# Kernel tuning notes

Measured on AMD Instinct MI355X. Metric: run time of the kernel, lower is better.

The kernel has to match this reference:

```python
import jax, jax.numpy as jnp
import numpy as np

DIM = 2048
ORDER = 4
L_MAX = 2048
BATCH = 4  # must equal ORDER due to broadcast in the original module
SEQ = 2048


def setup_inputs() -> dict:
    key = jax.random.key(0)
    k1, k2 = jax.random.split(key)
    x = jax.random.normal(k1, (BATCH, DIM, SEQ), dtype=jnp.float32)
    kernel = jax.random.normal(k2, (ORDER, DIM, L_MAX), dtype=jnp.float32) * 0.02
    bias = jnp.zeros((DIM,), dtype=jnp.float32)
    return {"x": x, "kernel": kernel, "bias": bias}


def reference(x, kernel, bias):
    # x: (B, dim, L); kernel: (order, dim, l_max); B == order by broadcast
    seq_len = x.shape[-1]
    n = 2 * seq_len  # zero-padded FFT length for linear (causal) convolution
    x_fft = jnp.fft.rfft(x, n=n, axis=-1)            # (B, dim, n//2+1) complex
    kernel_fft = jnp.fft.rfft(kernel, n=n, axis=-1)  # (order, dim, n//2+1)
    y_fft = x_fft * kernel_fft                       # broadcast: B == order
    y = jnp.fft.irfft(y_fft, n=n, axis=-1)[:, :, :seq_len]
    return y + x + bias[None, :, None]
```

## Files before the change

### kernel.cpp

```cpp
#include <hip/hip_runtime.h>

typedef __attribute__((ext_vector_type(8)))  short short8;
typedef __attribute__((ext_vector_type(16))) float f32x16;
typedef unsigned int uint;

#define SEQ   2048
#define KB0   1024
#define KSTR2 1040
#define KB1   (KB0 + KSTR2)
#define ZB    (KB0 + 2 * KSTR2)
#define LDSU  (ZB + 16)
#define EX0   1024
#define EX1   2048

__device__ inline uint pack2(float lo, float hi_) {
    uint ul = __float_as_uint(lo), uh = __float_as_uint(hi_);
    ul = (ul + 0x7fffu + ((ul >> 16) & 1u)) >> 16;
    uh = (uh + 0x7fffu + ((uh >> 16) & 1u)) >> 16;
    return (ul & 0xffffu) | (uh << 16);
}

__device__ inline int swz(int v) { return v ^ ((v >> 3) & 28); }

#define MFMA(A, B, C) __builtin_amdgcn_mfma_f32_32x32x16_bf16( \
    __builtin_bit_cast(short8, A), __builtin_bit_cast(short8, B), C, 0, 0, 0)

__global__ __launch_bounds__(128, 6)
void hyena_mfma(const float* __restrict__ x, const float* __restrict__ kern,
                const float* __restrict__ bias, float* __restrict__ out)
{
    __shared__ __align__(16) uint lds[LDSU];
    char* ldsb = (char*)lds;

    const int tid = threadIdx.x;
    const int wv  = tid >> 6;
    const int l   = tid & 63;
    const int n   = l & 31;
    const int hi  = l >> 5;
    const int row = blockIdx.x;
    const size_t rb = (size_t)row * SEQ;
    const float bv = bias[row & 2047];

    #pragma unroll
    for (int it = 0; it < 2; ++it) {
        const int e = it * 1024 + 8 * tid;
        float4 a = *(const float4*)&x[rb + e];
        float4 b = *(const float4*)&x[rb + e + 4];
        uint4 w = {pack2(a.x, a.y), pack2(a.z, a.w), pack2(b.x, b.y), pack2(b.z, b.w)};
        *(uint4*)&lds[swz(e >> 1)] = w;
    }
    #pragma unroll
    for (int it = 0; it < 2; ++it) {
        const int j = it * 1024 + 8 * tid;
        const float* kp0 = &kern[rb + (j == 2040 ? 0 : (2036 - j))];
        const float* kp1 = &kern[rb + (2040 - j)];
        float4 f0 = *(const float4*)kp0;
        float4 f1 = *(const float4*)kp1;
        float4 f2 = *(const float4*)(kp1 + 4);
        if (j == 2040) { f0.x = 0.f; f0.y = 0.f; f0.z = 0.f; f0.w = 0.f; }
        const float k0 = f2.w, k1 = f2.z, k2 = f2.y, k3 = f2.x;
        const float k4 = f1.w, k5 = f1.z, k6 = f1.y, k7 = f1.x;
        const float k8 = f0.w;
        const int m = j >> 1;
        uint4 w0 = {pack2(k0,k1), pack2(k2,k3), pack2(k4,k5), pack2(k6,k7)};
        uint4 w1 = {pack2(k1,k2), pack2(k3,k4), pack2(k5,k6), pack2(k7,k8)};
        *(uint4*)&lds[KB0 + m] = w0;
        *(uint4*)&lds[KB1 + m] = w1;
    }
    if (tid < 16) {
        lds[KB0 + 1024 + tid] = 0u;
        lds[KB1 + 1024 + tid] = 0u;
        lds[ZB + tid] = 0u;
    }
    __syncthreads();

    const int R0   = wv << 4;
    const int st00 = 2047 - n + 8 * hi;
    const int par  = st00 & 1;
    int kb  = (KB0 + par * KSTR2 + (st00 >> 1)) * 4 - 2048 - (R0 << 6);
    int kbh = kb + 2048;
    asm volatile("" : "+v"(kbh));
    int ua = 16 * n + 4 * hi - (R0 << 4);
    const int zb0 = ZB * 4 + 16 * hi;

    f32x16 acc0 = {}, acc1a = {}, acc1b = {};

    #pragma unroll 2
    for (int i = 0; i < 16; ++i) {
        const int r = R0 + i;
        const int b0  = swz(ua) * 4;
        const int b0s = swz(ua + 8) * 4;
        const int b1  = swz(ua + 512) * 4;
        const int b1s = swz(ua + 520) * 4;
        const int va0  = (n >= r) ? b0  : zb0;
        const int va0s = (n >= r) ? b0s : (zb0 + 32);
        uint4 a00 = *(const uint4*)(ldsb + va0);
        uint4 a01 = *(const uint4*)(ldsb + va0s);
        uint4 a10 = *(const uint4*)(ldsb + b1);
        uint4 a11 = *(const uint4*)(ldsb + b1s);

        const uint* kl = (const uint*)(ldsb + kb);
        const uint* kh = (const uint*)(ldsb + kbh);
        uint4 b00 = {kh[0], kh[1], kh[2],  kh[3]};
        uint4 b01 = {kh[8], kh[9], kh[10], kh[11]};
        uint4 b10 = {kl[0], kl[1], kl[2],  kl[3]};
        uint4 b11 = {kl[8], kl[9], kl[10], kl[11]};

        acc0  = MFMA(a00, b00, acc0);
        acc1a = MFMA(a10, b00, acc1a);
        acc0  = MFMA(a01, b01, acc0);
        acc1a = MFMA(a11, b01, acc1a);
        acc1b = MFMA(a00, b10, acc1b);
        acc1b = MFMA(a01, b11, acc1b);

        ua  -= 16;
        kb  -= 64;
        kbh -= 64;
    }
    __syncthreads();

    f32x16 part_send, part_keep;
    if (wv == 0) { part_send = acc1a + acc1b; part_keep = acc0; }
    else         { part_send = acc0;          part_keep = acc1a + acc1b; }
    const int exw = (wv == 0) ? EX0 : EX1;
    const int exr = (wv == 0) ? EX1 : EX0;
    #pragma unroll
    for (int q = 0; q < 4; ++q) {
        float4 f = {part_send[4*q], part_send[4*q+1], part_send[4*q+2], part_send[4*q+3]};
        *(float4*)&lds[exw + q * 256 + 4 * l] = f;
    }
    __syncthreads();
    f32x16 tile = part_keep;
    #pragma unroll
    for (int q = 0; q < 4; ++q) {
        float4 f = *(const float4*)&lds[exr + q * 256 + 4 * l];
        tile[4*q] += f.x; tile[4*q+1] += f.y; tile[4*q+2] += f.z; tile[4*q+3] += f.w;
    }

    #pragma unroll
    for (int t = 0; t < 16; ++t) {
        const int rloc = (t & 3) + 8 * (t >> 2) + 4 * hi;
        const int p = 32 * wv + rloc;
        const uint w = lds[swz(16 * p + (n >> 1))];
        const float xr = __uint_as_float((n & 1) ? (w & 0xffff0000u) : (w << 16));
        out[rb + (size_t)p * 32 + n] = tile[t] + xr + bv;
    }
}

extern "C" void kernel_launch(void* const* d_in, const int* in_sizes, int n_in,
                              void* d_out, int out_size, void* d_ws, size_t ws_size,
                              hipStream_t stream) {
    const float* x    = (const float*)d_in[0];
    const float* kern = (const float*)d_in[1];
    const float* bias = (const float*)d_in[2];
    float* out = (float*)d_out;

    hipLaunchKernelGGL(hyena_mfma, dim3(4 * 2048), dim3(128), 0, stream,
                       x, kern, bias, out);
}
```

Before: 60.50 us.

## Stage packed x row in global workspace and stream A operands via buffer loads

Adds a variant that writes the bf16-packed x row to a per-row global workspace instead of LDS. It then streams the MFMA A-operands with double-buffered buffer_load_dwordx4, using the buffer range check to supply zeros for out-of-range (causal-masked) rows. This is meant to shrink LDS usage and LDS read traffic so more blocks fit and the LDS pipe is relieved. The cost is a round trip through L2 for data that was just written, inline-asm waitcnt ordering, and a lower launch_bounds occupancy hint. The original LDS kernel is kept as a fallback when the workspace is too small.

```diff
diff --git a/kernel.cpp b/kernel.cpp
--- a/kernel.cpp
+++ b/kernel.cpp
@@ -3,15 +3,9 @@
 typedef __attribute__((ext_vector_type(8)))  short short8;
 typedef __attribute__((ext_vector_type(16))) float f32x16;
 typedef unsigned int uint;
-
-#define SEQ   2048
-#define KB0   1024
-#define KSTR2 1040
-#define KB1   (KB0 + KSTR2)
-#define ZB    (KB0 + 2 * KSTR2)
-#define LDSU  (ZB + 16)
-#define EX0   1024
-#define EX1   2048
+typedef __attribute__((ext_vector_type(4))) uint u32x4;
+
+#define SEQ 2048
 
 __device__ inline uint pack2(float lo, float hi_) {
     uint ul = __float_as_uint(lo), uh = __float_as_uint(hi_);
@@ -20,14 +14,19 @@
     return (ul & 0xffffu) | (uh << 16);
 }
 
-__device__ inline int swz(int v) { return v ^ ((v >> 3) & 28); }
-
 #define MFMA(A, B, C) __builtin_amdgcn_mfma_f32_32x32x16_bf16( \
     __builtin_bit_cast(short8, A), __builtin_bit_cast(short8, B), C, 0, 0, 0)
 
-__global__ __launch_bounds__(128, 6)
-void hyena_mfma(const float* __restrict__ x, const float* __restrict__ kern,
-                const float* __restrict__ bias, float* __restrict__ out)
+
+#define KSTR2 1040
+#define LDSU  2080
+#define EX0   0
+#define EX1   1024
+
+__global__ __launch_bounds__(128, 4)
+void hyena_vmem(const float* __restrict__ x, const float* __restrict__ kern,
+                const float* __restrict__ bias, float* __restrict__ out,
+                char* __restrict__ ws)
 {
     __shared__ __align__(16) uint lds[LDSU];
     char* ldsb = (char*)lds;
@@ -41,13 +40,173 @@
     const size_t rb = (size_t)row * SEQ;
     const float bv = bias[row & 2047];
 
+    char* wsrow = ws + (size_t)row * 4096;
+    u32x4 rsrc;
+    {
+        unsigned long long a = (unsigned long long)wsrow;
+        rsrc[0] = (uint)a; rsrc[1] = (uint)(a >> 32);
+        rsrc[2] = 4096u;   rsrc[3] = 0x00020000u;
+    }
+
+    #pragma unroll
+    for (int it = 0; it < 2; ++it) {
+        const int e = it * 1024 + 8 * tid;
+        float4 a = *(const float4*)&x[rb + e];
+        float4 b = *(const float4*)&x[rb + e + 4];
+        u32x4 w = {pack2(a.x, a.y), pack2(a.z, a.w), pack2(b.x, b.y), pack2(b.z, b.w)};
+        *(u32x4*)(wsrow + 2 * e) = w;
+    }
+    {
+        const int j = 8 * tid;
+        #pragma unroll
+        for (int it = 0; it < 2; ++it) {
+            const int jj = it * 1024 + j;
+            const float* kp0 = &kern[rb + (jj == 2040 ? 0 : (2036 - jj))];
+            const float* kp1 = &kern[rb + (2040 - jj)];
+            float4 f0 = *(const float4*)kp0;
+            float4 f1 = *(const float4*)kp1;
+            float4 f2 = *(const float4*)(kp1 + 4);
+            if (jj == 2040) { f0.x = 0.f; f0.y = 0.f; f0.z = 0.f; f0.w = 0.f; }
+            const float k0 = f2.w, k1 = f2.z, k2 = f2.y, k3 = f2.x;
+            const float k4 = f1.w, k5 = f1.z, k6 = f1.y, k7 = f1.x;
+            const float k8 = f0.w;
+            const int m = jj >> 1;
+            u32x4 w0 = {pack2(k0,k1), pack2(k2,k3), pack2(k4,k5), pack2(k6,k7)};
+            u32x4 w1 = {pack2(k1,k2), pack2(k3,k4), pack2(k5,k6), pack2(k7,k8)};
+            *(u32x4*)&lds[m]        = w0;
+            *(u32x4*)&lds[1040 + m] = w1;
+        }
+    }
+    if (tid < 16) {
+        lds[1024 + tid]        = 0u;
+        lds[1040 + 1024 + tid] = 0u;
+    }
+    asm volatile("s_waitcnt vmcnt(0)" ::: "memory");
+    __syncthreads();
+
+    const int R0   = wv << 4;
+    const int st00 = 2047 - n + 8 * hi;
+    const int par  = st00 & 1;
+    int kb  = (par * KSTR2 + (st00 >> 1)) * 4 - 2048 - (R0 << 6);
+    int kbh = kb + 2048;
+    asm volatile("" : "+v"(kbh));
+    uint voff0 = (uint)(64 * (n - R0) + 16 * hi);
+    uint voff1 = voff0 + 2048u;
+
+    f32x16 acc0 = {}, acc1a = {}, acc1b = {};
+    u32x4 A00[2], A01[2], A10[2], A11[2];
+
+    #define ISSUE_A(buf, v0, v1)                                                     \
+        asm volatile("buffer_load_dwordx4 %0, %1, %2, 0 offen"                       \
+                     : "=v"(A00[buf]) : "v"(v0), "s"(rsrc));                         \
+        asm volatile("buffer_load_dwordx4 %0, %1, %2, 0 offen offset:32"             \
+                     : "=v"(A01[buf]) : "v"(v0), "s"(rsrc));                         \
+        asm volatile("buffer_load_dwordx4 %0, %1, %2, 0 offen"                       \
+                     : "=v"(A10[buf]) : "v"(v1), "s"(rsrc));                         \
+        asm volatile("buffer_load_dwordx4 %0, %1, %2, 0 offen offset:32"             \
+                     : "=v"(A11[buf]) : "v"(v1), "s"(rsrc));
+
+    ISSUE_A(0, voff0, voff1)
+
+    #pragma unroll
+    for (int i = 0; i < 16; ++i) {
+        const int cur = i & 1, nxt = cur ^ 1;
+        if (i < 15) {
+            voff0 -= 64u; voff1 -= 64u;
+            ISSUE_A(nxt, voff0, voff1)
+            asm volatile("s_waitcnt vmcnt(4)");
+        } else {
+            asm volatile("s_waitcnt vmcnt(0)");
+        }
+        __builtin_amdgcn_sched_barrier(0);
+
+        const uint* kl = (const uint*)(ldsb + kb);
+        const uint* kh = (const uint*)(ldsb + kbh);
+        u32x4 b00 = {kh[0], kh[1], kh[2],  kh[3]};
+        u32x4 b01 = {kh[8], kh[9], kh[10], kh[11]};
+        u32x4 b10 = {kl[0], kl[1], kl[2],  kl[3]};
+        u32x4 b11 = {kl[8], kl[9], kl[10], kl[11]};
+
+        acc0  = MFMA(A00[cur], b00, acc0);
+        acc1a = MFMA(A10[cur], b00, acc1a);
+        acc0  = MFMA(A01[cur], b01, acc0);
+        acc1a = MFMA(A11[cur], b01, acc1a);
+        acc1b = MFMA(A00[cur], b10, acc1b);
+        acc1b = MFMA(A01[cur], b11, acc1b);
+
+        kb -= 64; kbh -= 64;
+    }
+    __syncthreads();
+
+    f32x16 part_send, part_keep;
+    if (wv == 0) { part_send = acc1a + acc1b; part_keep = acc0; }
+    else         { part_send = acc0;          part_keep = acc1a + acc1b; }
+    const int exw = (wv == 0) ? EX0 : EX1;
+    const int exr = (wv == 0) ? EX1 : EX0;
+    #pragma unroll
+    for (int q = 0; q < 4; ++q) {
+        float4 f = {part_send[4*q], part_send[4*q+1], part_send[4*q+2], part_send[4*q+3]};
+        *(float4*)&lds[exw + q * 256 + 4 * l] = f;
+    }
+    __syncthreads();
+    f32x16 tile = part_keep;
+    #pragma unroll
+    for (int q = 0; q < 4; ++q) {
+        float4 f = *(const float4*)&lds[exr + q * 256 + 4 * l];
+        tile[4*q] += f.x; tile[4*q+1] += f.y; tile[4*q+2] += f.z; tile[4*q+3] += f.w;
+    }
+
+    uint xr16[16];
+    const uint voffr = (uint)(2048 * wv + 256 * hi + 2 * n);
+    #define LOADR(t)                                                              \
+        asm volatile("buffer_load_ushort %0, %1, %2, 0 offen offset:%3"           \
+                     : "=v"(xr16[t]) : "v"(voffr), "s"(rsrc),                     \
+                       "i"(64 * (((t) & 3) + 8 * ((t) >> 2))));
+    LOADR(0)  LOADR(1)  LOADR(2)  LOADR(3)  LOADR(4)  LOADR(5)  LOADR(6)  LOADR(7)
+    LOADR(8)  LOADR(9)  LOADR(10) LOADR(11) LOADR(12) LOADR(13) LOADR(14) LOADR(15)
+    asm volatile("s_waitcnt vmcnt(0)");
+    __builtin_amdgcn_sched_barrier(0);
+
+    #pragma unroll
+    for (int t = 0; t < 16; ++t) {
+        const int rloc = (t & 3) + 8 * (t >> 2) + 4 * hi;
+        const int p = 32 * wv + rloc;
+        const float xr = __uint_as_float(xr16[t] << 16);
+        out[rb + (size_t)p * 32 + n] = tile[t] + xr + bv;
+    }
+}
+
+#define KB0f   1024
+#define KSTR2f 1040
+#define KB1f   (KB0f + KSTR2f)
+#define ZBf    (KB0f + 2 * KSTR2f)
+#define LDSUf  (ZBf + 16)
+
+__device__ inline int swzf(int v) { return v ^ ((v >> 3) & 28); }
+
+__global__ __launch_bounds__(128, 6)
+void hyena_lds(const float* __restrict__ x, const float* __restrict__ kern,
+               const float* __restrict__ bias, float* __restrict__ out)
+{
+    __shared__ __align__(16) uint lds[LDSUf];
+    char* ldsb = (char*)lds;
+
+    const int tid = threadIdx.x;
+    const int wv  = tid >> 6;
+    const int l   = tid & 63;
+    const int n   = l & 31;
+    const int hi  = l >> 5;
+    const int row = blockIdx.x;
+    const size_t rb = (size_t)row * SEQ;
+    const float bv = bias[row & 2047];
+
     #pragma unroll
     for (int it = 0; it < 2; ++it) {
         const int e = it * 1024 + 8 * tid;
         float4 a = *(const float4*)&x[rb + e];
         float4 b = *(const float4*)&x[rb + e + 4];
         uint4 w = {pack2(a.x, a.y), pack2(a.z, a.w), pack2(b.x, b.y), pack2(b.z, b.w)};
-        *(uint4*)&lds[swz(e >> 1)] = w;
+        *(uint4*)&lds[swzf(e >> 1)] = w;
     }
     #pragma unroll
     for (int it = 0; it < 2; ++it) {
@@ -64,34 +223,34 @@
         const int m = j >> 1;
         uint4 w0 = {pack2(k0,k1), pack2(k2,k3), pack2(k4,k5), pack2(k6,k7)};
         uint4 w1 = {pack2(k1,k2), pack2(k3,k4), pack2(k5,k6), pack2(k7,k8)};
-        *(uint4*)&lds[KB0 + m] = w0;
-        *(uint4*)&lds[KB1 + m] = w1;
+        *(uint4*)&lds[KB0f + m] = w0;
+        *(uint4*)&lds[KB1f + m] = w1;
     }
     if (tid < 16) {
-        lds[KB0 + 1024 + tid] = 0u;
-        lds[KB1 + 1024 + tid] = 0u;
-        lds[ZB + tid] = 0u;
+        lds[KB0f + 1024 + tid] = 0u;
+        lds[KB1f + 1024 + tid] = 0u;
+        lds[ZBf + tid] = 0u;
     }
     __syncthreads();
 
     const int R0   = wv << 4;
     const int st00 = 2047 - n + 8 * hi;
     const int par  = st00 & 1;
-    int kb  = (KB0 + par * KSTR2 + (st00 >> 1)) * 4 - 2048 - (R0 << 6);
+    int kb  = (KB0f + par * KSTR2f + (st00 >> 1)) * 4 - 2048 - (R0 << 6);
     int kbh = kb + 2048;
     asm volatile("" : "+v"(kbh));
     int ua = 16 * n + 4 * hi - (R0 << 4);
-    const int zb0 = ZB * 4 + 16 * hi;
+    const int zb0 = ZBf * 4 + 16 * hi;
 
     f32x16 acc0 = {}, acc1a = {}, acc1b = {};
 
     #pragma unroll 2
     for (int i = 0; i < 16; ++i) {
         const int r = R0 + i;
-        const int b0  = swz(ua) * 4;
-        const int b0s = swz(ua + 8) * 4;
-        const int b1  = swz(ua + 512) * 4;
-        const int b1s = swz(ua + 520) * 4;
+        const int b0  = swzf(ua) * 4;
+        const int b0s = swzf(ua + 8) * 4;
+        const int b1  = swzf(ua + 512) * 4;
+        const int b1s = swzf(ua + 520) * 4;
         const int va0  = (n >= r) ? b0  : zb0;
         const int va0s = (n >= r) ? b0s : (zb0 + 32);
         uint4 a00 = *(const uint4*)(ldsb + va0);
@@ -113,17 +272,15 @@
         acc1b = MFMA(a00, b10, acc1b);
         acc1b = MFMA(a01, b11, acc1b);
 
-        ua  -= 16;
-        kb  -= 64;
-        kbh -= 64;
+        ua  -= 16; kb -= 64; kbh -= 64;
     }
     __syncthreads();
 
     f32x16 part_send, part_keep;
     if (wv == 0) { part_send = acc1a + acc1b; part_keep = acc0; }
     else         { part_send = acc0;          part_keep = acc1a + acc1b; }
-    const int exw = (wv == 0) ? EX0 : EX1;
-    const int exr = (wv == 0) ? EX1 : EX0;
+    const int exw = (wv == 0) ? 1024 : 2048;
+    const int exr = (wv == 0) ? 2048 : 1024;
     #pragma unroll
     for (int q = 0; q < 4; ++q) {
         float4 f = {part_send[4*q], part_send[4*q+1], part_send[4*q+2], part_send[4*q+3]};
@@ -141,7 +298,7 @@
     for (int t = 0; t < 16; ++t) {
         const int rloc = (t & 3) + 8 * (t >> 2) + 4 * hi;
         const int p = 32 * wv + rloc;
-        const uint w = lds[swz(16 * p + (n >> 1))];
+        const uint w = lds[swzf(16 * p + (n >> 1))];
         const float xr = __uint_as_float((n & 1) ? (w & 0xffff0000u) : (w << 16));
         out[rb + (size_t)p * 32 + n] = tile[t] + xr + bv;
     }
@@ -155,6 +312,12 @@
     const float* bias = (const float*)d_in[2];
     float* out = (float*)d_out;
 
-    hipLaunchKernelGGL(hyena_mfma, dim3(4 * 2048), dim3(128), 0, stream,
-                       x, kern, bias, out);
+    const size_t need = (size_t)8192 * 4096;
+    if (ws_size >= need) {
+        hipLaunchKernelGGL(hyena_vmem, dim3(8192), dim3(128), 0, stream,
+                           x, kern, bias, out, (char*)d_ws);
+    } else {
+        hipLaunchKernelGGL(hyena_lds, dim3(8192), dim3(128), 0, stream,
+                           x, kern, bias, out);
+    }
 }
```

Measured after the change: 76.86 us. +27.1%, slower.
